# Kernel tuning notes

Measured on AMD Instinct MI355X. Metric: run time of the kernel, lower is better.

The kernel has to match this reference:

```python
import jax, jax.numpy as jnp
import numpy as np

B, C, H, W = 2, 72, 96, 96
FACTOR = 4  # input_dim // output_dim = 72 // 18


def setup_inputs() -> dict:
    key = jax.random.key(0)
    ks = jax.random.split(key, 7)
    s = 1.0 / np.sqrt(C)
    return {
        "x": jax.random.normal(ks[0], (B, C, H, W), dtype=jnp.float32),
        "Wq": jax.random.normal(ks[1], (C, C), dtype=jnp.float32) * s,
        "bq": jax.random.normal(ks[2], (C,), dtype=jnp.float32) * 0.01,
        "Wk": jax.random.normal(ks[3], (C, C), dtype=jnp.float32) * s,
        "bk": jax.random.normal(ks[4], (C,), dtype=jnp.float32) * 0.01,
        "Wv": jax.random.normal(ks[5], (C, C), dtype=jnp.float32) * s,
        "bv": jax.random.normal(ks[6], (C,), dtype=jnp.float32) * 0.01,
    }


def reference(x, Wq, bq, Wk, bk, Wv, bv):
    b, c, h, w = x.shape
    n = h * w
    flat = x.reshape(b, c, n)  # [B, C, N]
    # 1x1 convs == per-pixel channel matmuls
    q = jnp.einsum('dc,bcn->bdn', Wq, flat) + bq[None, :, None]
    k = jnp.einsum('dc,bcn->bdn', Wk, flat) + bk[None, :, None]
    v = jnp.einsum('dc,bcn->bdn', Wv, flat) + bv[None, :, None]
    # scores[b,i,j] = sum_c q[b,c,i] * k[b,c,j]  (no 1/sqrt(d) scaling, as in source)
    scores = jnp.einsum('bci,bcj->bij', q, k)  # [B, N, N]
    attn = jax.nn.softmax(scores, axis=-1)
    # weighted_values = bmm(v, attn^T): wv[b,c,i] = sum_j v[b,c,j] * attn[b,i,j]
    wv = jnp.einsum('bcj,bij->bci', v, attn)  # [B, C, N]
    wv = wv.reshape(b, c // FACTOR, FACTOR, h, w)
    xg = x.reshape(b, c // FACTOR, FACTOR, h, w)
    pooled = jnp.sum(xg * wv, axis=2)  # [B, C//FACTOR, H, W]
    return pooled
```

## Files before the change

### kernel.cpp

```cpp
#include <hip/hip_runtime.h>

#define NPIX 9216
#define CIN 72
#define CP 96
#define SPLITS 8
#define JCHUNK (NPIX / SPLITS)
#define JTILES (JCHUNK / 64)
#define L2E   1.44269504088896f
#define EXPB  46.1662413084468f

typedef __attribute__((ext_vector_type(8))) short bf16x8;
typedef __attribute__((ext_vector_type(8))) _Float16 f16x8;
typedef __attribute__((ext_vector_type(4))) float f32x4;

#define MFMA_BF16(A,B,C) __builtin_amdgcn_mfma_f32_16x16x32_bf16(A,B,C,0,0,0)
#define MFMA_F16(A,B,C)  __builtin_amdgcn_mfma_f32_16x16x32_f16(A,B,C,0,0,0)

static __device__ __forceinline__ unsigned short f2bf(float f) {
  unsigned u = __float_as_uint(f);
  u += 0x7fffu + ((u >> 16) & 1u);
  return (unsigned short)(u >> 16);
}
static __device__ __forceinline__ float bf2f(unsigned short h) {
  return __uint_as_float(((unsigned)h) << 16);
}
static __device__ __forceinline__ unsigned short f2h(float f) {
  _Float16 h = (_Float16)f;
  return *(unsigned short*)&h;
}
static __device__ __forceinline__ unsigned pack_bf_trunc(float lo, float hi) {
  return (__float_as_uint(lo) >> 16) | (__float_as_uint(hi) & 0xffff0000u);
}
static __device__ __forceinline__ void load_lds16(const unsigned short* g,
                                                  unsigned short* l) {
  __builtin_amdgcn_global_load_lds(
      (const __attribute__((address_space(1))) unsigned int*)g,
      (__attribute__((address_space(3))) unsigned int*)l, 16, 0, 0);
}

__global__ __launch_bounds__(256) void wprep_kernel(
    const float* __restrict__ Wq, const float* __restrict__ Wk,
    const float* __restrict__ Wv,
    unsigned short* __restrict__ WH, unsigned short* __restrict__ WL)
{
  int id = blockIdx.x * 256 + threadIdx.x;
  if (id >= 3 * 80 * 96) return;
  int mat = id / (80 * 96);
  int rem = id % (80 * 96);
  int d = rem / 96, c = rem % 96;
  const float* W = (mat == 0) ? Wq : (mat == 1) ? Wk : Wv;
  float v = (d < 72 && c < 72) ? W[d * 72 + c] : 0.f;
  unsigned short hi = f2bf(v);
  WH[id] = hi;
  WL[id] = f2bf(v - bf2f(hi));
}

#define XTS 104

__global__ __launch_bounds__(192) void qkv_kernel(
    const float* __restrict__ x,
    const unsigned short* __restrict__ WH, const unsigned short* __restrict__ WL,
    const float* __restrict__ bq, const float* __restrict__ bk,
    const float* __restrict__ bv,
    unsigned short* __restrict__ QH, unsigned short* __restrict__ KH,
    unsigned short* __restrict__ VG)
{
  __shared__ __align__(16) unsigned short xth[16 * XTS];
  __shared__ __align__(16) unsigned short xtl[16 * XTS];
  __shared__ __align__(16) unsigned short obuf[2][16 * XTS];

  const int t    = threadIdx.x;
  const int w    = t >> 6;
  const int lane = t & 63;
  const int quad = lane >> 4;
  const int l15  = lane & 15;
  const int bid  = blockIdx.x;
  const int b    = bid / 576;
  const int n0   = (bid % 576) * 16;

  for (int e = t; e < 288; e += 192) {
    int c = e >> 2, f4 = (e & 3) * 4;
    float4 xv = *(const float4*)(x + ((size_t)b * CIN + c) * NPIX + n0 + f4);
    float vv[4] = {xv.x, xv.y, xv.z, xv.w};
#pragma unroll
    for (int k = 0; k < 4; ++k) {
      unsigned short hi = f2bf(vv[k]);
      xth[(f4 + k) * XTS + c] = hi;
      xtl[(f4 + k) * XTS + c] = f2bf(vv[k] - bf2f(hi));
    }
  }
  for (int e = t; e < 24 * 16; e += 192) {
    int c = 72 + (e >> 4), px = e & 15;
    xth[px * XTS + c] = 0;
    xtl[px * XTS + c] = 0;
  }
  __syncthreads();

  bf16x8 xbh[3], xbl[3];
#pragma unroll
  for (int ks = 0; ks < 3; ++ks) {
    int off = l15 * XTS + ks * 32 + quad * 8;
    xbh[ks] = *(const bf16x8*)(xth + off);
    xbl[ks] = *(const bf16x8*)(xtl + off);
  }

  const unsigned short* wh = WH + w * 80 * 96;
  const unsigned short* wl = WL + w * 80 * 96;
  const float* bias = (w == 0) ? bq : (w == 1) ? bk : bv;

  f32x4 acc[5];
#pragma unroll
  for (int dm = 0; dm < 5; ++dm) {
    acc[dm] = (f32x4){0.f, 0.f, 0.f, 0.f};
#pragma unroll
    for (int ks = 0; ks < 3; ++ks) {
      bf16x8 ah = *(const bf16x8*)(wh + (dm * 16 + l15) * 96 + ks * 32 + quad * 8);
      bf16x8 al = *(const bf16x8*)(wl + (dm * 16 + l15) * 96 + ks * 32 + quad * 8);
      acc[dm] = MFMA_BF16(ah, xbh[ks], acc[dm]);
      acc[dm] = MFMA_BF16(ah, xbl[ks], acc[dm]);
      acc[dm] = MFMA_BF16(al, xbh[ks], acc[dm]);
    }
  }

  if (w < 2) {
    unsigned short* ob = obuf[w];
#pragma unroll
    for (int dm = 0; dm < 5; ++dm)
#pragma unroll
      for (int r = 0; r < 4; ++r) {
        int d = dm * 16 + quad * 4 + r;
        float v = acc[dm][r] + (d < 72 ? bias[d] : 0.f);
        ob[l15 * XTS + d] = f2h(v);
      }
    unsigned short* outp = (w == 0) ? QH : KH;
    const size_t obase = ((size_t)b * NPIX + n0) * CP;
    uint4 z; z.x = z.y = z.z = z.w = 0u;
    for (int f = lane; f < 192; f += 64) {
      int row = f / 12, col = f % 12;
      *(uint4*)(outp + obase + (size_t)row * CP + col * 8) =
          (col < 10) ? *(const uint4*)(ob + row * XTS + col * 8) : z;
    }
  } else {
#pragma unroll
    for (int dm = 0; dm < 5; ++dm)
#pragma unroll
      for (int r = 0; r < 4; ++r) {
        int d = dm * 16 + quad * 4 + r;
        float v = (d < 72) ? acc[dm][r] + bias[d] : (d == 72 ? 1.0f : 0.f);
        VG[((size_t)b * 80 + d) * NPIX + n0 + l15] = f2bf(v);
      }
  }
}

#define KSP 96
#define VSP 72
#define PSP 72

__global__ __launch_bounds__(256, 3) void flash_kernel(
    const float* __restrict__ x,
    const unsigned short* __restrict__ QH, const unsigned short* __restrict__ KH,
    const unsigned short* __restrict__ VG,
    float* __restrict__ NUM, float* __restrict__ LPART)
{
  __shared__ __align__(16) unsigned short ls_kh[64 * KSP];
  __shared__ __align__(16) unsigned short ls_vs[80 * VSP];
  __shared__ __align__(16) unsigned short ps[4][48 * PSP];

  const int t    = threadIdx.x;
  const int w    = t >> 6;
  const int lane = t & 63;
  const int quad = lane >> 4;
  const int l15  = lane & 15;

  const int bid  = blockIdx.x;
  const int sp   = bid & 7;
  const int slot = bid >> 3;
  const int b    = slot / 48;
  const int it   = slot % 48;
  const int i0w  = it * 192 + w * 48;

  f16x8 qh[3][3];
#pragma unroll
  for (int mi = 0; mi < 3; ++mi)
#pragma unroll
    for (int ks = 0; ks < 3; ++ks) {
      size_t off = ((size_t)b * NPIX + i0w + mi * 16 + l15) * CP + ks * 32 + quad * 8;
      qh[mi][ks] = *(const f16x8*)(QH + off);
    }

  f32x4 oacc[3][5];
#pragma unroll
  for (int mi = 0; mi < 3; ++mi)
#pragma unroll
    for (int nt = 0; nt < 5; ++nt) oacc[mi][nt] = (f32x4){0.f, 0.f, 0.f, 0.f};

  unsigned short* psw = ps[w];

  const unsigned short* kpg = KH + ((size_t)b * NPIX + sp * JCHUNK) * CP;
  const unsigned short* vpg = VG + (size_t)b * 80 * NPIX + sp * JCHUNK;

  for (int jt = 0; jt < JTILES; ++jt, kpg += 64 * CP, vpg += 64) {
#pragma unroll
    for (int k = 0; k < 3; ++k) {
      int chunk = w + k * 4;
      load_lds16(kpg + chunk * 512 + lane * 8, ls_kh + chunk * 512);
    }
    for (int idx = t; idx < 640; idx += 256) {
      int r = idx >> 3, c = idx & 7;
      *(uint4*)(ls_vs + r * VSP + c * 8) =
          *(const uint4*)(vpg + (size_t)r * NPIX + c * 8);
    }
    __syncthreads();

#pragma unroll
    for (int tj = 0; tj < 4; ++tj) {
      f16x8 fkh[3];
#pragma unroll
      for (int ks = 0; ks < 3; ++ks)
        fkh[ks] = *(const f16x8*)(ls_kh + (tj * 16 + l15) * KSP + ks * 32 + quad * 8);
#pragma unroll
      for (int mi = 0; mi < 3; ++mi) {
        f32x4 s = (f32x4){0.f, 0.f, 0.f, 0.f};
        s = MFMA_F16(fkh[0], qh[mi][0], s);
        s = MFMA_F16(fkh[1], qh[mi][1], s);
        s = MFMA_F16(fkh[2], qh[mi][2], s);
        float p0 = __builtin_amdgcn_exp2f(__builtin_fmaf(s[0], L2E, -EXPB));
        float p1 = __builtin_amdgcn_exp2f(__builtin_fmaf(s[1], L2E, -EXPB));
        float p2 = __builtin_amdgcn_exp2f(__builtin_fmaf(s[2], L2E, -EXPB));
        float p3 = __builtin_amdgcn_exp2f(__builtin_fmaf(s[3], L2E, -EXPB));
        uint2 pk;
        pk.x = pack_bf_trunc(p0, p1);
        pk.y = pack_bf_trunc(p2, p3);
        *(uint2*)(psw + (mi * 16 + l15) * PSP + tj * 16 + quad * 4) = pk;
      }
    }

#pragma unroll
    for (int js = 0; js < 2; ++js) {
      bf16x8 pf[3];
#pragma unroll
      for (int mi = 0; mi < 3; ++mi)
        pf[mi] = *(const bf16x8*)(psw + (mi * 16 + l15) * PSP + js * 32 + quad * 8);
#pragma unroll
      for (int nt = 0; nt < 5; ++nt) {
        bf16x8 vf = *(const bf16x8*)(ls_vs + (nt * 16 + l15) * VSP + js * 32 + quad * 8);
#pragma unroll
        for (int mi = 0; mi < 3; ++mi)
          oacc[mi][nt] = MFMA_BF16(vf, pf[mi], oacc[mi][nt]);
      }
    }
    __syncthreads();
  }

  const size_t sb = (size_t)(sp * 2 + b);
#pragma unroll
  for (int mi = 0; mi < 3; ++mi) {
    const int i = i0w + mi * 16 + l15;
    if (quad == 2)
      LPART[sb * NPIX + i] = oacc[mi][4][0];
#pragma unroll
    for (int nt = 0; nt < 5; ++nt) {
      int c0 = nt * 16 + quad * 4;
      if (c0 < 72) {
        float num = 0.f;
#pragma unroll
        for (int r = 0; r < 4; ++r)
          num = __builtin_fmaf(x[((size_t)b * CIN + c0 + r) * NPIX + i],
                               oacc[mi][nt][r], num);
        NUM[(sb * 18 + (c0 >> 2)) * NPIX + i] = num;
      }
    }
  }
}

__global__ __launch_bounds__(256) void combine_pool_kernel(
    const float* __restrict__ NUM, const float* __restrict__ LPART,
    float* __restrict__ out)
{
  int id = blockIdx.x * 256 + threadIdx.x;
  if (id >= 2 * 18 * (NPIX / 4)) return;
  int n = (id % (NPIX / 4)) * 4;
  int rest = id / (NPIX / 4);
  int g = rest % 18, b = rest / 18;

  float4 A = make_float4(0.f, 0.f, 0.f, 0.f);
  float4 L = make_float4(0.f, 0.f, 0.f, 0.f);
#pragma unroll
  for (int s = 0; s < SPLITS; ++s) {
    size_t sb = (size_t)(s * 2 + b);
    float4 a = *(const float4*)(NUM + (sb * 18 + g) * NPIX + n);
    float4 l = *(const float4*)(LPART + sb * NPIX + n);
    A.x += a.x; A.y += a.y; A.z += a.z; A.w += a.w;
    L.x += l.x; L.y += l.y; L.z += l.z; L.w += l.w;
  }
  float4 r;
  r.x = A.x / L.x; r.y = A.y / L.y; r.z = A.z / L.z; r.w = A.w / L.w;
  *(float4*)(out + (size_t)id * 4) = r;
}

extern "C" void kernel_launch(void* const* d_in, const int* in_sizes, int n_in,
                              void* d_out, int out_size, void* d_ws, size_t ws_size,
                              hipStream_t stream) {
  const float* x  = (const float*)d_in[0];
  const float* Wq = (const float*)d_in[1];
  const float* bq = (const float*)d_in[2];
  const float* Wk = (const float*)d_in[3];
  const float* bk = (const float*)d_in[4];
  const float* Wv = (const float*)d_in[5];
  const float* bv = (const float*)d_in[6];
  float* out = (float*)d_out;

  char* p = (char*)d_ws;
  const size_t szQK = (size_t)2 * NPIX * CP * 2;
  unsigned short* QH = (unsigned short*)p; p += szQK;
  unsigned short* KH = (unsigned short*)p; p += szQK;
  unsigned short* VG = (unsigned short*)p; p += (size_t)2 * 80 * NPIX * 2;
  unsigned short* WH = (unsigned short*)p; p += (size_t)3 * 80 * 96 * 2;
  unsigned short* WL = (unsigned short*)p; p += (size_t)3 * 80 * 96 * 2;
  float* NUM = (float*)p; p += (size_t)SPLITS * 2 * 18 * NPIX * 4;
  float* LPART = (float*)p; p += (size_t)SPLITS * 2 * NPIX * 4;

  wprep_kernel<<<(3 * 80 * 96 + 255) / 256, 256, 0, stream>>>(Wq, Wk, Wv, WH, WL);
  qkv_kernel<<<1152, 192, 0, stream>>>(x, WH, WL, bq, bk, bv, QH, KH, VG);
  flash_kernel<<<768, 256, 0, stream>>>(x, QH, KH, VG, NUM, LPART);
  combine_pool_kernel<<<(2 * 18 * (NPIX / 4) + 255) / 256, 256, 0, stream>>>(
      NUM, LPART, out);
}
```

Baseline: 150.5 us.

## Persist QKV weights in registers, pipeline x staging, and XOR-swizzle flash LDS tiles

The QKV projection kernel now handles 64 pixels per block: it loads the split-bf16 weights and biases into registers once and double-buffers the x tiles into LDS with direct global-to-LDS loads, so the next tile loads while the current one is computed. The flash kernel replaces padded LDS strides for the K tile and the P scratch buffer with an XOR swizzle, to cut bank conflicts while keeping tiles unpadded. In exchange the QKV kernel uses many more registers (launch bounds 192,1) and launches far fewer blocks, which may reduce parallelism.

```diff
diff --git a/kernel.cpp b/kernel.cpp
--- a/kernel.cpp
+++ b/kernel.cpp
@@ -31,8 +31,7 @@
 static __device__ __forceinline__ unsigned pack_bf_trunc(float lo, float hi) {
   return (__float_as_uint(lo) >> 16) | (__float_as_uint(hi) & 0xffff0000u);
 }
-static __device__ __forceinline__ void load_lds16(const unsigned short* g,
-                                                  unsigned short* l) {
+static __device__ __forceinline__ void load_lds16(const void* g, void* l) {
   __builtin_amdgcn_global_load_lds(
       (const __attribute__((address_space(1))) unsigned int*)g,
       (__attribute__((address_space(3))) unsigned int*)l, 16, 0, 0);
@@ -56,8 +55,21 @@
 }
 
 #define XTS 104
-
-__global__ __launch_bounds__(192) void qkv_kernel(
+#define QS  4
+
+static __device__ __forceinline__ void stage_x(const float* __restrict__ x,
+    float* lbuf, int b, int n0, int w, int lane) {
+#pragma unroll
+  for (int kk = 0; kk < 2; ++kk) {
+    const int ch = w * 2 + kk;
+    const int r = ch * 16 + (lane >> 2);
+    const int c = (r < 72) ? r : 71;
+    const float* src = x + ((size_t)b * CIN + c) * NPIX + n0 + (lane & 3) * 4;
+    load_lds16(src, lbuf + ch * 256);
+  }
+}
+
+__global__ __launch_bounds__(192, 1) void qkv_kernel(
     const float* __restrict__ x,
     const unsigned short* __restrict__ WH, const unsigned short* __restrict__ WL,
     const float* __restrict__ bq, const float* __restrict__ bk,
@@ -65,8 +77,7 @@
     unsigned short* __restrict__ QH, unsigned short* __restrict__ KH,
     unsigned short* __restrict__ VG)
 {
-  __shared__ __align__(16) unsigned short xth[16 * XTS];
-  __shared__ __align__(16) unsigned short xtl[16 * XTS];
+  __shared__ __align__(16) float ls_x[2][6 * 256];
   __shared__ __align__(16) unsigned short obuf[2][16 * XTS];
 
   const int t    = threadIdx.x;
@@ -75,86 +86,96 @@
   const int quad = lane >> 4;
   const int l15  = lane & 15;
   const int bid  = blockIdx.x;
-  const int b    = bid / 576;
-  const int n0   = (bid % 576) * 16;
-
-  for (int e = t; e < 288; e += 192) {
-    int c = e >> 2, f4 = (e & 3) * 4;
-    float4 xv = *(const float4*)(x + ((size_t)b * CIN + c) * NPIX + n0 + f4);
-    float vv[4] = {xv.x, xv.y, xv.z, xv.w};
-#pragma unroll
-    for (int k = 0; k < 4; ++k) {
-      unsigned short hi = f2bf(vv[k]);
-      xth[(f4 + k) * XTS + c] = hi;
-      xtl[(f4 + k) * XTS + c] = f2bf(vv[k] - bf2f(hi));
-    }
-  }
-  for (int e = t; e < 24 * 16; e += 192) {
-    int c = 72 + (e >> 4), px = e & 15;
-    xth[px * XTS + c] = 0;
-    xtl[px * XTS + c] = 0;
-  }
-  __syncthreads();
-
-  bf16x8 xbh[3], xbl[3];
-#pragma unroll
-  for (int ks = 0; ks < 3; ++ks) {
-    int off = l15 * XTS + ks * 32 + quad * 8;
-    xbh[ks] = *(const bf16x8*)(xth + off);
-    xbl[ks] = *(const bf16x8*)(xtl + off);
-  }
+  const int b    = bid / 144;
+  const int g0   = bid % 144;
+  const int nbase = g0 * 64;
 
   const unsigned short* wh = WH + w * 80 * 96;
   const unsigned short* wl = WL + w * 80 * 96;
+  bf16x8 WAh[5][3], WAl[5][3];
+#pragma unroll
+  for (int dm = 0; dm < 5; ++dm)
+#pragma unroll
+    for (int ks = 0; ks < 3; ++ks) {
+      WAh[dm][ks] = *(const bf16x8*)(wh + (dm * 16 + l15) * 96 + ks * 32 + quad * 8);
+      WAl[dm][ks] = *(const bf16x8*)(wl + (dm * 16 + l15) * 96 + ks * 32 + quad * 8);
+    }
   const float* bias = (w == 0) ? bq : (w == 1) ? bk : bv;
-
-  f32x4 acc[5];
-#pragma unroll
-  for (int dm = 0; dm < 5; ++dm) {
-    acc[dm] = (f32x4){0.f, 0.f, 0.f, 0.f};
+  float bs[5][4];
+#pragma unroll
+  for (int dm = 0; dm < 5; ++dm)
+#pragma unroll
+    for (int r = 0; r < 4; ++r) {
+      int d = dm * 16 + quad * 4 + r;
+      bs[dm][r] = (d < 72) ? bias[d] : 0.f;
+    }
+
+  stage_x(x, ls_x[0], b, nbase, w, lane);
+  __syncthreads();
+
+  for (int s = 0; s < QS; ++s) {
+    const int n0 = nbase + s * 16;
+    if (s + 1 < QS) stage_x(x, ls_x[(s + 1) & 1], b, n0 + 16, w, lane);
+    const float* lx = ls_x[s & 1];
+
+    bf16x8 xbh[3], xbl[3];
 #pragma unroll
     for (int ks = 0; ks < 3; ++ks) {
-      bf16x8 ah = *(const bf16x8*)(wh + (dm * 16 + l15) * 96 + ks * 32 + quad * 8);
-      bf16x8 al = *(const bf16x8*)(wl + (dm * 16 + l15) * 96 + ks * 32 + quad * 8);
-      acc[dm] = MFMA_BF16(ah, xbh[ks], acc[dm]);
-      acc[dm] = MFMA_BF16(ah, xbl[ks], acc[dm]);
-      acc[dm] = MFMA_BF16(al, xbh[ks], acc[dm]);
-    }
-  }
-
-  if (w < 2) {
-    unsigned short* ob = obuf[w];
-#pragma unroll
-    for (int dm = 0; dm < 5; ++dm)
-#pragma unroll
-      for (int r = 0; r < 4; ++r) {
-        int d = dm * 16 + quad * 4 + r;
-        float v = acc[dm][r] + (d < 72 ? bias[d] : 0.f);
-        ob[l15 * XTS + d] = f2h(v);
-      }
-    unsigned short* outp = (w == 0) ? QH : KH;
-    const size_t obase = ((size_t)b * NPIX + n0) * CP;
-    uint4 z; z.x = z.y = z.z = z.w = 0u;
-    for (int f = lane; f < 192; f += 64) {
-      int row = f / 12, col = f % 12;
-      *(uint4*)(outp + obase + (size_t)row * CP + col * 8) =
-          (col < 10) ? *(const uint4*)(ob + row * XTS + col * 8) : z;
-    }
-  } else {
-#pragma unroll
-    for (int dm = 0; dm < 5; ++dm)
-#pragma unroll
-      for (int r = 0; r < 4; ++r) {
-        int d = dm * 16 + quad * 4 + r;
-        float v = (d < 72) ? acc[dm][r] + bias[d] : (d == 72 ? 1.0f : 0.f);
-        VG[((size_t)b * 80 + d) * NPIX + n0 + l15] = f2bf(v);
-      }
-  }
-}
-
-#define KSP 96
+#pragma unroll
+      for (int j = 0; j < 8; ++j) {
+        float v = lx[(ks * 32 + quad * 8 + j) * 16 + l15];
+        unsigned short hi = f2bf(v);
+        ((unsigned short*)&xbh[ks])[j] = hi;
+        ((unsigned short*)&xbl[ks])[j] = f2bf(v - bf2f(hi));
+      }
+    }
+
+    f32x4 acc[5];
+#pragma unroll
+    for (int dm = 0; dm < 5; ++dm) {
+      acc[dm] = (f32x4){0.f, 0.f, 0.f, 0.f};
+#pragma unroll
+      for (int ks = 0; ks < 3; ++ks) {
+        acc[dm] = MFMA_BF16(WAh[dm][ks], xbh[ks], acc[dm]);
+        acc[dm] = MFMA_BF16(WAh[dm][ks], xbl[ks], acc[dm]);
+        acc[dm] = MFMA_BF16(WAl[dm][ks], xbh[ks], acc[dm]);
+      }
+    }
+
+    if (w < 2) {
+      unsigned short* ob = obuf[w];
+#pragma unroll
+      for (int dm = 0; dm < 5; ++dm)
+#pragma unroll
+        for (int r = 0; r < 4; ++r) {
+          int d = dm * 16 + quad * 4 + r;
+          float v = acc[dm][r] + bs[dm][r];
+          ob[l15 * XTS + d] = f2h(v);
+        }
+      unsigned short* outp = (w == 0) ? QH : KH;
+      const size_t obase = ((size_t)b * NPIX + n0) * CP;
+      uint4 z; z.x = z.y = z.z = z.w = 0u;
+      for (int f = lane; f < 192; f += 64) {
+        int row = f / 12, col = f % 12;
+        *(uint4*)(outp + obase + (size_t)row * CP + col * 8) =
+            (col < 10) ? *(const uint4*)(ob + row * XTS + col * 8) : z;
+      }
+    } else {
+#pragma unroll
+      for (int dm = 0; dm < 5; ++dm)
+#pragma unroll
+        for (int r = 0; r < 4; ++r) {
+          int d = dm * 16 + quad * 4 + r;
+          float v = (d < 72) ? acc[dm][r] + bs[dm][r] : (d == 72 ? 1.0f : 0.f);
+          VG[((size_t)b * 80 + d) * NPIX + n0 + l15] = f2bf(v);
+        }
+    }
+    __syncthreads();
+  }
+}
+
+#define KSP 128
 #define VSP 72
-#define PSP 72
 
 __global__ __launch_bounds__(256, 3) void flash_kernel(
     const float* __restrict__ x,
@@ -164,7 +185,7 @@
 {
   __shared__ __align__(16) unsigned short ls_kh[64 * KSP];
   __shared__ __align__(16) unsigned short ls_vs[80 * VSP];
-  __shared__ __align__(16) unsigned short ps[4][48 * PSP];
+  __shared__ __align__(16) unsigned short ps[4][48 * 64];
 
   const int t    = threadIdx.x;
   const int w    = t >> 6;
@@ -195,15 +216,19 @@
     for (int nt = 0; nt < 5; ++nt) oacc[mi][nt] = (f32x4){0.f, 0.f, 0.f, 0.f};
 
   unsigned short* psw = ps[w];
+  const int swz = l15 & 7;
 
   const unsigned short* kpg = KH + ((size_t)b * NPIX + sp * JCHUNK) * CP;
   const unsigned short* vpg = VG + (size_t)b * 80 * NPIX + sp * JCHUNK;
 
   for (int jt = 0; jt < JTILES; ++jt, kpg += 64 * CP, vpg += 64) {
 #pragma unroll
-    for (int k = 0; k < 3; ++k) {
+    for (int k = 0; k < 4; ++k) {
       int chunk = w + k * 4;
-      load_lds16(kpg + chunk * 512 + lane * 8, ls_kh + chunk * 512);
+      int r  = chunk * 4 + (lane >> 4);
+      int lu = (lane & 15) ^ (r & 7);
+      int su = (lu < 12) ? lu : 0;
+      load_lds16(kpg + r * CP + su * 8, ls_kh + chunk * 512);
     }
     for (int idx = t; idx < 640; idx += 256) {
       int r = idx >> 3, c = idx & 7;
@@ -214,10 +239,11 @@
 
 #pragma unroll
     for (int tj = 0; tj < 4; ++tj) {
+      const int krow = tj * 16 + l15;
       f16x8 fkh[3];
 #pragma unroll
       for (int ks = 0; ks < 3; ++ks)
-        fkh[ks] = *(const f16x8*)(ls_kh + (tj * 16 + l15) * KSP + ks * 32 + quad * 8);
+        fkh[ks] = *(const f16x8*)(ls_kh + krow * KSP + (((ks * 4 + quad) ^ swz) << 3));
 #pragma unroll
       for (int mi = 0; mi < 3; ++mi) {
         f32x4 s = (f32x4){0.f, 0.f, 0.f, 0.f};
@@ -231,7 +257,8 @@
         uint2 pk;
         pk.x = pack_bf_trunc(p0, p1);
         pk.y = pack_bf_trunc(p2, p3);
-        *(uint2*)(psw + (mi * 16 + l15) * PSP + tj * 16 + quad * 4) = pk;
+        int pu = (tj * 2 + (quad >> 1)) ^ swz;
+        *(uint2*)(psw + (mi * 16 + l15) * 64 + (pu << 3) + (quad & 1) * 4) = pk;
       }
     }
 
@@ -240,7 +267,8 @@
       bf16x8 pf[3];
 #pragma unroll
       for (int mi = 0; mi < 3; ++mi)
-        pf[mi] = *(const bf16x8*)(psw + (mi * 16 + l15) * PSP + js * 32 + quad * 8);
+        pf[mi] = *(const bf16x8*)(psw + (mi * 16 + l15) * 64 +
+                                  ((((js << 2) + quad) ^ swz) << 3));
 #pragma unroll
       for (int nt = 0; nt < 5; ++nt) {
         bf16x8 vf = *(const bf16x8*)(ls_vs + (nt * 16 + l15) * VSP + js * 32 + quad * 8);
@@ -321,7 +349,7 @@
   float* LPART = (float*)p; p += (size_t)SPLITS * 2 * NPIX * 4;
 
   wprep_kernel<<<(3 * 80 * 96 + 255) / 256, 256, 0, stream>>>(Wq, Wk, Wv, WH, WL);
-  qkv_kernel<<<1152, 192, 0, stream>>>(x, WH, WL, bq, bk, bv, QH, KH, VG);
+  qkv_kernel<<<288, 192, 0, stream>>>(x, WH, WL, bq, bk, bv, QH, KH, VG);
   flash_kernel<<<768, 256, 0, stream>>>(x, QH, KH, VG, NUM, LPART);
   combine_pool_kernel<<<(2 * 18 * (NPIX / 4) + 255) / 256, 256, 0, stream>>>(
       NUM, LPART, out);
```

After: 150.7 us. No clear change (+0.1%).
